# Kernel tuning notes

Hardware: AMD Instinct MI355X
Metric: run time of the kernel (lower is better)

Reference implementation:

```python
import jax, jax.numpy as jnp
import numpy as np

NEG_INF = -1.0e9


def setup_inputs() -> dict:
    key = jax.random.key(0)
    ks = jax.random.split(key, 7)
    B, D, L, N, K = 4096, 512, 20, 8192, 64
    return {
        "inputs_embed": jax.random.normal(ks[0], (B, D), jnp.float32),
        "labels_embed": jax.random.normal(ks[1], (B, D), jnp.float32),
        "labels": jax.random.normal(ks[2], (B, L), jnp.float32),
        "all_labels_embed": jax.random.normal(ks[3], (N, D), jnp.float32),
        "all_labels": jax.random.normal(ks[4], (N, L), jnp.float32),
        "neg_ids_in": jax.random.randint(ks[5], (B, K), 0, B, jnp.int32),
        "neg_ids_lb": jax.random.randint(ks[6], (B, K), 0, N, jnp.int32),
    }


def reference(inputs_embed, labels_embed, labels, all_labels_embed, all_labels,
              neg_ids_in, neg_ids_lb):
    # --- negative sampling (indices supplied; equals tf.gather of tiled table) ---
    neg_ie = inputs_embed[neg_ids_in]        # [B,K,D] negatives from inputs
    neg_le = all_labels_embed[neg_ids_lb]    # [B,K,D] negatives from label table
    # bad-negative masks: negative label features identical to the positive's
    bad_in = jnp.all(labels[neg_ids_in] == labels[:, None, :], axis=-1).astype(inputs_embed.dtype)      # [B,K]
    bad_lb = jnp.all(all_labels[neg_ids_lb] == labels[:, None, :], axis=-1).astype(inputs_embed.dtype)  # [B,K]

    # --- similarities (dot products) ---
    sim_pos = jnp.sum(inputs_embed * labels_embed, axis=-1, keepdims=True)            # [B,1]
    sim_neg_il = jnp.einsum("bd,bkd->bk", inputs_embed, neg_le) + NEG_INF * bad_lb    # [B,K]
    sim_neg_ll = jnp.einsum("bd,bkd->bk", labels_embed, neg_le) + NEG_INF * bad_lb
    sim_neg_ii = jnp.einsum("bd,bkd->bk", inputs_embed, neg_ie) + NEG_INF * bad_in
    sim_neg_li = jnp.einsum("bd,bkd->bk", labels_embed, neg_ie) + NEG_INF * bad_in

    # --- accuracy ---
    max_all = jnp.max(jnp.concatenate([sim_pos, sim_neg_il], axis=-1), axis=-1)
    acc = jnp.mean((max_all == sim_pos[:, 0]).astype(jnp.float32))

    # --- softmax loss, correct class at index 0 ---
    logits = jnp.concatenate([sim_pos, sim_neg_il, sim_neg_ll, sim_neg_ii, sim_neg_li], axis=-1)  # [B,1+4K]
    per_ex = -jax.nn.log_softmax(logits, axis=-1)[:, 0]   # [B]

    # --- confidence-based loss scaling: loss_scale(-per_ex) ---
    q = jnp.exp(-per_ex)
    scale = jnp.where(jnp.max(q) > 0.5,
                      jax.lax.stop_gradient(((1.0 - q) / 0.5) ** 4),
                      jnp.ones_like(q))
    loss = jnp.mean(per_ex * scale)
    return loss, acc
```

## Files before the change

### kernel.cpp

```cpp
#include <hip/hip_runtime.h>
#include <hip/hip_bf16.h>

#define BB 4096
#define DD 512
#define LLAB 20
#define NN 8192
#define KK 64

constexpr float kNegInf = -1.0e9f;
constexpr float kLn2 = 0.69314718055994530942f;
constexpr float kWlPe = 2.5f;
constexpr float kWlTie = 2.0f;

#define OFF_STATS 16384
#define OFF_WL    16640
#define OFF_HLAB  33280
#define OFF_HAL   66048
#define OFF_SIE   131584
#define OFF_SALE  147968
#define OFF_IEQ   180736
#define OFF_ALEQ  (OFF_IEQ + (size_t)BB * DD)
#define WS_NEED   (OFF_ALEQ + (size_t)NN * DD)

__device__ __forceinline__ float dot4(const float4& a, const float4& b) {
  return a.x * b.x + a.y * b.y + a.z * b.z + a.w * b.w;
}

__device__ __forceinline__ float waveReduceSum(float v) {
#pragma unroll
  for (int s = 1; s < 64; s <<= 1) v += __shfl_xor(v, s);
  return v;
}

__device__ __forceinline__ float waveReduceMax(float v) {
#pragma unroll
  for (int s = 1; s < 64; s <<= 1) v = fmaxf(v, __shfl_xor(v, s));
  return v;
}

__device__ __forceinline__ float waveReduceMin(float v) {
#pragma unroll
  for (int s = 1; s < 64; s <<= 1) v = fminf(v, __shfl_xor(v, s));
  return v;
}

__device__ __forceinline__ unsigned long long hash20(const float* __restrict__ p) {
  unsigned long long h = 1469598103934665603ull;
#pragma unroll
  for (int t = 0; t < LLAB; ++t) {
    h ^= (unsigned long long)__float_as_uint(p[t]);
    h *= 1099511628211ull;
  }
  return h;
}

__device__ __forceinline__ int sdot4i(unsigned a, unsigned b, int acc) {
#if __has_builtin(__builtin_amdgcn_sdot4)
  return __builtin_amdgcn_sdot4((int)a, (int)b, acc, false);
#else
#pragma unroll
  for (int t = 0; t < 4; ++t)
    acc += (int)(signed char)(a >> (8 * t)) * (int)(signed char)(b >> (8 * t));
  return acc;
#endif
}

__device__ __forceinline__ unsigned pk4i8(float a, float b, float c, float d, float inv) {
  const int q0 = (int)rintf(a * inv);
  const int q1 = (int)rintf(b * inv);
  const int q2 = (int)rintf(c * inv);
  const int q3 = (int)rintf(d * inv);
  return (q0 & 255) | ((q1 & 255) << 8) | ((q2 & 255) << 16) | ((q3 & 255) << 24);
}

__device__ __forceinline__ float max8abs(const float4& a, const float4& c) {
  return fmaxf(fmaxf(fmaxf(fabsf(a.x), fabsf(a.y)), fmaxf(fabsf(a.z), fabsf(a.w))),
               fmaxf(fmaxf(fabsf(c.x), fabsf(c.y)), fmaxf(fabsf(c.z), fabsf(c.w))));
}

__global__ void init_kernel(unsigned* stats) {
  if (threadIdx.x == 0) {
    stats[0] = 0u;
    stats[1] = 0u;
  }
}

__global__ __launch_bounds__(256) void prep_kernel(
    const float* __restrict__ ie, const float* __restrict__ ale,
    const float* __restrict__ labels, const float* __restrict__ al,
    char* __restrict__ ie_q, char* __restrict__ ale_q,
    float* __restrict__ s_ie, float* __restrict__ s_ale,
    unsigned long long* __restrict__ h_lab,
    unsigned long long* __restrict__ h_al, unsigned* __restrict__ stats) {
  const int tid = threadIdx.x;
  const int lane = tid & 63;
  const int wave = tid >> 6;
  const int w = blockIdx.x * 4 + wave;

  const float* src;
  char* dst;
  float* sc;
  int row;
  if (w < BB) {
    src = ie; dst = ie_q; sc = s_ie; row = w;
  } else {
    src = ale; dst = ale_q; sc = s_ale; row = w - BB;
  }

  const float4* r4 = (const float4*)(src + (size_t)row * DD);
  const float4 a = r4[2 * lane], c = r4[2 * lane + 1];
  float mx = waveReduceMax(max8abs(a, c));
  mx = fmaxf(mx, 1e-20f);
  const float inv = 127.0f / mx;
  uint2 o;
  o.x = pk4i8(a.x, a.y, a.z, a.w, inv);
  o.y = pk4i8(c.x, c.y, c.z, c.w, inv);
  ((uint2*)(dst + (size_t)row * DD))[lane] = o;
  if (lane == 0) sc[row] = mx * (1.0f / 127.0f);

  const int g = blockIdx.x * 256 + tid;
  if (g == 0) {
    stats[0] = 0u;
    stats[1] = 0u;
  }
  if (g < BB) h_lab[g] = hash20(labels + (size_t)g * LLAB);
  else if (g < BB + NN) h_al[g - BB] = hash20(al + (size_t)(g - BB) * LLAB);
}

__global__ __launch_bounds__(256, 4) void row_i8_kernel(
    const float* __restrict__ ie, const float* __restrict__ le,
    const char* __restrict__ ie_q, const char* __restrict__ ale_q,
    const float* __restrict__ s_ie, const float* __restrict__ s_ale,
    const unsigned long long* __restrict__ h_lab,
    const unsigned long long* __restrict__ h_al,
    const int* __restrict__ nin, const int* __restrict__ nlb,
    float* __restrict__ per_ex, int* __restrict__ wl,
    unsigned* __restrict__ stats) {
  const int b = blockIdx.x;
  const int tid = threadIdx.x;
  const int lane = tid & 63;
  const int wave = tid >> 6;
  const int c = lane & 3;
  const int g = lane >> 2;

  __shared__ unsigned qs[2][144];
  __shared__ float qsc[2];
  __shared__ float sims[1 + 4 * KK];
  __shared__ float wred[8];

  const int wuni = __builtin_amdgcn_readfirstlane(wave);
  const int k = wuni * 16 + g;

  const int jl = nlb[b * KK + k];
  const int ji = nin[b * KK + k];
  const unsigned long long hb = h_lab[b];
  const bool bad_lb = (h_al[jl] == hb);
  const bool bad_in = (h_lab[ji] == hb);
  const float sA = s_ale[jl];
  const float sB = s_ie[ji];

  const uint4* arow = (const uint4*)(ale_q + (size_t)jl * DD);
  const uint4* brow = (const uint4*)(ie_q + (size_t)ji * DD);
  uint4 Ar[8], Br[8];
#pragma unroll
  for (int i = 0; i < 8; ++i) {
    Ar[i] = arow[i * 4 + c];
    Br[i] = brow[i * 4 + c];
  }

  if (wave == 0) {
    const float4* ie4 = (const float4*)(ie + (size_t)b * DD);
    const float4* le4 = (const float4*)(le + (size_t)b * DD);
    const float4 qi0 = ie4[2 * lane], qi1 = ie4[2 * lane + 1];
    const float4 ql0 = le4[2 * lane], ql1 = le4[2 * lane + 1];
    float p = dot4(qi0, ql0) + dot4(qi1, ql1);
    p = waveReduceSum(p);
    if (lane == 0) sims[0] = p;
    const float ami = fmaxf(waveReduceMax(max8abs(qi0, qi1)), 1e-20f);
    const float aml = fmaxf(waveReduceMax(max8abs(ql0, ql1)), 1e-20f);
    const float inv_i = 127.0f / ami, inv_l = 127.0f / aml;
    if (lane == 0) {
      qsc[0] = ami * (1.0f / 127.0f);
      qsc[1] = aml * (1.0f / 127.0f);
    }
    const int cw = (lane >> 1) & 3, iw = lane >> 3;
    const int woff = cw * 36 + iw * 4 + (lane & 1) * 2;
    qs[0][woff] = pk4i8(qi0.x, qi0.y, qi0.z, qi0.w, inv_i);
    qs[0][woff + 1] = pk4i8(qi1.x, qi1.y, qi1.z, qi1.w, inv_i);
    qs[1][woff] = pk4i8(ql0.x, ql0.y, ql0.z, ql0.w, inv_l);
    qs[1][woff + 1] = pk4i8(ql1.x, ql1.y, ql1.z, ql1.w, inv_l);
  }
  __syncthreads();

  int il = 0, ll = 0, ii = 0, li = 0;
#pragma unroll
  for (int i = 0; i < 8; ++i) {
    const uint4 qi = *(const uint4*)&qs[0][c * 36 + i * 4];
    const uint4 ql = *(const uint4*)&qs[1][c * 36 + i * 4];
    il = sdot4i(Ar[i].x, qi.x, il); il = sdot4i(Ar[i].y, qi.y, il);
    il = sdot4i(Ar[i].z, qi.z, il); il = sdot4i(Ar[i].w, qi.w, il);
    ll = sdot4i(Ar[i].x, ql.x, ll); ll = sdot4i(Ar[i].y, ql.y, ll);
    ll = sdot4i(Ar[i].z, ql.z, ll); ll = sdot4i(Ar[i].w, ql.w, ll);
    ii = sdot4i(Br[i].x, qi.x, ii); ii = sdot4i(Br[i].y, qi.y, ii);
    ii = sdot4i(Br[i].z, qi.z, ii); ii = sdot4i(Br[i].w, qi.w, ii);
    li = sdot4i(Br[i].x, ql.x, li); li = sdot4i(Br[i].y, ql.y, li);
    li = sdot4i(Br[i].z, ql.z, li); li = sdot4i(Br[i].w, ql.w, li);
  }

  const bool odd = (lane & 1) != 0;
  const int x = odd ? il : ii;
  const int y = odd ? ll : li;
  const int rx = __shfl_xor(x, 1);
  const int ry = __shfl_xor(y, 1);
  const int aa = (odd ? ii : il) + rx;
  const int bb = (odd ? li : ll) + ry;
  const bool hi2 = (lane & 2) != 0;
  const int s1 = hi2 ? aa : bb;
  const int r1 = __shfl_xor(s1, 2);
  const int vi = (hi2 ? bb : aa) + r1;

  const float srow = (c & 1) ? sB : sA;
  const float sq = (c & 2) ? qsc[1] : qsc[0];
  const float v = (float)vi * (srow * sq);
  const bool badf = (c & 1) ? bad_in : bad_lb;
  const float s = badf ? v + kNegInf : v;
  const int slot = ((c & 1) << 1) | (c >> 1);
  sims[1 + slot * KK + k] = s;
  __syncthreads();

  const float vv = sims[1 + tid];
  const float s0 = sims[0];
  float wmax = waveReduceMax(vv);
  if (lane == 0) wred[wave] = wmax;
  __syncthreads();
  float m = fmaxf(fmaxf(wred[0], wred[1]), fmaxf(wred[2], wred[3]));
  m = fmaxf(m, s0);
  const float e = expf(vv - m);
  float wsum = waveReduceSum(e);
  if (lane == 0) wred[4 + wave] = wsum;
  __syncthreads();
  if (tid == 0) {
    const float tot = wred[4] + wred[5] + wred[6] + wred[7] + expf(s0 - m);
    const float pe = m + logf(tot) - s0;
    per_ex[b] = pe;
    const float max_il = wred[0];
    const bool wl_row = (pe < kWlPe) || (fabsf(s0 - max_il) < kWlTie);
    if (wl_row) {
      const unsigned p = atomicAdd(&stats[1], 1u);
      wl[p] = b;
    } else if (s0 >= max_il) {
      atomicAdd(&stats[0], 1u);
    }
  }
}

__device__ __forceinline__ void row_f32_body(
    int b, const float* __restrict__ ie, const float* __restrict__ le,
    const float* __restrict__ labels, const float* __restrict__ ale,
    const float* __restrict__ al, const int* __restrict__ nin,
    const int* __restrict__ nlb, float* __restrict__ per_ex,
    unsigned* __restrict__ stats, bool count_acc, float* sims, float* wred) {
  const int tid = threadIdx.x;
  const int lane = tid & 63;
  const int wave = tid >> 6;

  const float4* ie4 = (const float4*)(ie + (size_t)b * DD);
  const float4* le4 = (const float4*)(le + (size_t)b * DD);
  float4 ier0 = ie4[lane], ier1 = ie4[lane + 64];
  float4 ler0 = le4[lane], ler1 = le4[lane + 64];
  float lab = (lane < LLAB) ? labels[(size_t)b * LLAB + lane] : 0.0f;

  if (wave == 0) {
    float p = dot4(ier0, ler0) + dot4(ier1, ler1);
    p = waveReduceSum(p);
    if (lane == 0) sims[0] = p;
  }

#pragma unroll 2
  for (int kk = 0; kk < KK / 4; ++kk) {
    const int k = wave * (KK / 4) + kk;
    const int j_lb = __builtin_amdgcn_readfirstlane(nlb[(size_t)b * KK + k]);
    const int j_in = __builtin_amdgcn_readfirstlane(nin[(size_t)b * KK + k]);

    const float4* rle = (const float4*)(ale + (size_t)j_lb * DD);
    const float4* rie = (const float4*)(ie + (size_t)j_in * DD);
    float4 vle0 = rle[lane], vle1 = rle[lane + 64];
    float4 vie0 = rie[lane], vie1 = rie[lane + 64];

    bool ein = true, elb = true;
    if (lane < LLAB) {
      ein = (labels[(size_t)j_in * LLAB + lane] == lab);
      elb = (al[(size_t)j_lb * LLAB + lane] == lab);
    }
    const bool bad_in = (__ballot(ein) == ~0ull);
    const bool bad_lb = (__ballot(elb) == ~0ull);

    float a_il = dot4(vle0, ier0) + dot4(vle1, ier1);
    float a_ll = dot4(vle0, ler0) + dot4(vle1, ler1);
    float a_ii = dot4(vie0, ier0) + dot4(vie1, ier1);
    float a_li = dot4(vie0, ler0) + dot4(vie1, ler1);

    const bool oddl = (lane & 1) != 0;
    float sx = oddl ? a_il : a_ii;
    float sy = oddl ? a_ll : a_li;
    float rx = __shfl_xor(sx, 1);
    float ry = __shfl_xor(sy, 1);
    float mx = (oddl ? a_ii : a_il) + rx;
    float my = (oddl ? a_li : a_ll) + ry;
    const bool hi2 = (lane & 2) != 0;
    float s1 = hi2 ? mx : my;
    float r1 = __shfl_xor(s1, 2);
    float v = (hi2 ? my : mx) + r1;
    v += __shfl_xor(v, 4);
    v += __shfl_xor(v, 8);
    v += __shfl_xor(v, 16);
    v += __shfl_xor(v, 32);

    if (lane < 4) {
      const bool badf = (lane & 1) ? bad_in : bad_lb;
      const float s = badf ? v + kNegInf : v;
      const int slot = ((lane & 1) << 1) | ((lane >> 1) & 1);
      sims[1 + slot * KK + k] = s;
    }
  }
  __syncthreads();

  const float v = sims[1 + tid];
  const float s0 = sims[0];
  float wmax = waveReduceMax(v);
  if (lane == 0) wred[wave] = wmax;
  __syncthreads();
  float m = fmaxf(fmaxf(wred[0], wred[1]), fmaxf(wred[2], wred[3]));
  m = fmaxf(m, s0);
  const float e = expf(v - m);
  float wsum = waveReduceSum(e);
  if (lane == 0) wred[4 + wave] = wsum;
  __syncthreads();
  if (tid == 0) {
    const float tot = wred[4] + wred[5] + wred[6] + wred[7] + expf(s0 - m);
    per_ex[b] = m + logf(tot) - s0;
    if (count_acc) {
      const float max_il = wred[0];
      if (s0 >= max_il) atomicAdd(&stats[0], 1u);
    }
  }
}

__global__ __launch_bounds__(256) void row_f32_kernel(
    const float* __restrict__ ie, const float* __restrict__ le,
    const float* __restrict__ labels, const float* __restrict__ ale,
    const float* __restrict__ al, const int* __restrict__ nin,
    const int* __restrict__ nlb, float* __restrict__ per_ex,
    unsigned* __restrict__ stats) {
  __shared__ float sims[1 + 4 * KK];
  __shared__ float wred[8];
  row_f32_body(blockIdx.x, ie, le, labels, ale, al, nin, nlb, per_ex, stats,
               true, sims, wred);
}

__global__ __launch_bounds__(256) void fixup_kernel(
    const float* __restrict__ ie, const float* __restrict__ le,
    const float* __restrict__ labels, const float* __restrict__ ale,
    const float* __restrict__ al, const int* __restrict__ nin,
    const int* __restrict__ nlb, float* __restrict__ per_ex,
    const int* __restrict__ wl, unsigned* __restrict__ stats) {
  __shared__ float sims[1 + 4 * KK];
  __shared__ float wred[8];
  const int n = (int)stats[1];
  for (int w = blockIdx.x; w < n; w += gridDim.x) {
    row_f32_body(wl[w], ie, le, labels, ale, al, nin, nlb, per_ex, stats,
                 true, sims, wred);
    __syncthreads();
  }
}

__global__ __launch_bounds__(256) void finalize_kernel(
    const float* __restrict__ per_ex, const unsigned* __restrict__ stats,
    float* __restrict__ out) {
  __shared__ float pe_s[BB];
  __shared__ float wred[8];
  const int tid = threadIdx.x;
  const int lane = tid & 63;
  const int wave = tid >> 6;

  float mn = 1.0e30f;
#pragma unroll 4
  for (int i = tid; i < BB; i += 256) {
    const float v = per_ex[i];
    pe_s[i] = v;
    mn = fminf(mn, v);
  }
  mn = waveReduceMin(mn);
  if (lane == 0) wred[wave] = mn;
  __syncthreads();
  const float minpe = fminf(fminf(wred[0], wred[1]), fminf(wred[2], wred[3]));
  const bool scale_on = (minpe < kLn2);
  __syncthreads();

  float sum = 0.0f;
#pragma unroll 4
  for (int i = tid; i < BB; i += 256) {
    const float pe = pe_s[i];
    float s = 1.0f;
    if (scale_on) {
      const float q = expf(-pe);
      const float t = 2.0f * (1.0f - q);
      const float t2 = t * t;
      s = t2 * t2;
    }
    sum += pe * s;
  }
  sum = waveReduceSum(sum);
  if (lane == 0) wred[4 + wave] = sum;
  __syncthreads();
  if (tid == 0) {
    const float tot = wred[4] + wred[5] + wred[6] + wred[7];
    out[0] = tot / (float)BB;
    out[1] = (float)stats[0] / (float)BB;
  }
}

extern "C" void kernel_launch(void* const* d_in, const int* in_sizes, int n_in,
                              void* d_out, int out_size, void* d_ws, size_t ws_size,
                              hipStream_t stream) {
  const float* ie = (const float*)d_in[0];
  const float* le = (const float*)d_in[1];
  const float* labels = (const float*)d_in[2];
  const float* ale = (const float*)d_in[3];
  const float* al = (const float*)d_in[4];
  const int* nin = (const int*)d_in[5];
  const int* nlb = (const int*)d_in[6];
  float* out = (float*)d_out;

  float* per_ex = (float*)d_ws;
  unsigned* stats = (unsigned*)((char*)d_ws + OFF_STATS);
  int* wl = (int*)((char*)d_ws + OFF_WL);

  if (ws_size >= WS_NEED) {
    char* ie_q = (char*)d_ws + OFF_IEQ;
    char* ale_q = (char*)d_ws + OFF_ALEQ;
    float* s_ie = (float*)((char*)d_ws + OFF_SIE);
    float* s_ale = (float*)((char*)d_ws + OFF_SALE);
    unsigned long long* h_lab = (unsigned long long*)((char*)d_ws + OFF_HLAB);
    unsigned long long* h_al = (unsigned long long*)((char*)d_ws + OFF_HAL);
    const int prep_blocks = (BB + NN) / 4;
    hipLaunchKernelGGL(prep_kernel, dim3(prep_blocks), dim3(256), 0, stream,
                       ie, ale, labels, al, ie_q, ale_q, s_ie, s_ale,
                       h_lab, h_al, stats);
    hipLaunchKernelGGL(row_i8_kernel, dim3(BB), dim3(256), 0, stream,
                       ie, le, ie_q, ale_q, s_ie, s_ale, h_lab, h_al,
                       nin, nlb, per_ex, wl, stats);
    hipLaunchKernelGGL(fixup_kernel, dim3(64), dim3(256), 0, stream,
                       ie, le, labels, ale, al, nin, nlb, per_ex, wl, stats);
  } else {
    hipLaunchKernelGGL(init_kernel, dim3(1), dim3(64), 0, stream, stats);
    hipLaunchKernelGGL(row_f32_kernel, dim3(BB), dim3(256), 0, stream,
                       ie, le, labels, ale, al, nin, nlb, per_ex, stats);
  }
  hipLaunchKernelGGL(finalize_kernel, dim3(1), dim3(256), 0, stream,
                     per_ex, stats, out);
}
```

Measured before the change: 58.21 us.

## Precompute query quantization in prep and fuse f32 fixup into row kernel

Moves the per-row positive dot product and the int8 quantization of inputs and labels embeddings into the prep kernel, so the row kernel only loads prequantized query rows into shared memory. It also drops one sims shared-memory round trip by reducing max and sum straight from registers. The separate fixup kernel and its worklist atomics go away, and uncertain rows now run the exact f32 path inline within the same block. This saves a launch and a serial tail, but a block that hits the fixup path gets slower and the extra code may raise register pressure in the row kernel.

Result: faster. 53.29 us (-8.5%).

```diff
diff --git a/kernel.cpp b/kernel.cpp
--- a/kernel.cpp
+++ b/kernel.cpp
@@ -13,13 +13,15 @@
 constexpr float kWlTie = 2.0f;
 
 #define OFF_STATS 16384
-#define OFF_WL    16640
-#define OFF_HLAB  33280
-#define OFF_HAL   66048
-#define OFF_SIE   131584
-#define OFF_SALE  147968
-#define OFF_IEQ   180736
-#define OFF_ALEQ  (OFF_IEQ + (size_t)BB * DD)
+#define OFF_SP    16640
+#define OFF_SIE   33024
+#define OFF_SLE   49408
+#define OFF_SALE  65792
+#define OFF_HLAB  98560
+#define OFF_HAL   131328
+#define OFF_IEQ   196864
+#define OFF_LEQ   2294016
+#define OFF_ALEQ  4391168
 #define WS_NEED   (OFF_ALEQ + (size_t)NN * DD)
 
 __device__ __forceinline__ float dot4(const float4& a, const float4& b) {
@@ -79,17 +81,16 @@
 }
 
 __global__ void init_kernel(unsigned* stats) {
-  if (threadIdx.x == 0) {
-    stats[0] = 0u;
-    stats[1] = 0u;
-  }
+  if (threadIdx.x == 0) stats[0] = 0u;
 }
 
 __global__ __launch_bounds__(256) void prep_kernel(
-    const float* __restrict__ ie, const float* __restrict__ ale,
-    const float* __restrict__ labels, const float* __restrict__ al,
-    char* __restrict__ ie_q, char* __restrict__ ale_q,
-    float* __restrict__ s_ie, float* __restrict__ s_ale,
+    const float* __restrict__ ie, const float* __restrict__ le,
+    const float* __restrict__ ale, const float* __restrict__ labels,
+    const float* __restrict__ al, char* __restrict__ ie_q,
+    char* __restrict__ le_q, char* __restrict__ ale_q,
+    float* __restrict__ s_ie, float* __restrict__ s_le,
+    float* __restrict__ s_ale, float* __restrict__ sp,
     unsigned long long* __restrict__ h_lab,
     unsigned long long* __restrict__ h_al, unsigned* __restrict__ stats) {
   const int tid = threadIdx.x;
@@ -97,161 +98,47 @@
   const int wave = tid >> 6;
   const int w = blockIdx.x * 4 + wave;
 
-  const float* src;
-  char* dst;
-  float* sc;
-  int row;
   if (w < BB) {
-    src = ie; dst = ie_q; sc = s_ie; row = w;
+    const float4* i4 = (const float4*)(ie + (size_t)w * DD);
+    const float4* l4 = (const float4*)(le + (size_t)w * DD);
+    const float4 a0 = i4[2 * lane], a1 = i4[2 * lane + 1];
+    const float4 b0 = l4[2 * lane], b1 = l4[2 * lane + 1];
+    float p = dot4(a0, b0) + dot4(a1, b1);
+    p = waveReduceSum(p);
+    float mi = fmaxf(waveReduceMax(max8abs(a0, a1)), 1e-20f);
+    const float inv_i = 127.0f / mi;
+    uint2 oi;
+    oi.x = pk4i8(a0.x, a0.y, a0.z, a0.w, inv_i);
+    oi.y = pk4i8(a1.x, a1.y, a1.z, a1.w, inv_i);
+    ((uint2*)(ie_q + (size_t)w * DD))[lane] = oi;
+    float ml = fmaxf(waveReduceMax(max8abs(b0, b1)), 1e-20f);
+    const float inv_l = 127.0f / ml;
+    uint2 ol;
+    ol.x = pk4i8(b0.x, b0.y, b0.z, b0.w, inv_l);
+    ol.y = pk4i8(b1.x, b1.y, b1.z, b1.w, inv_l);
+    ((uint2*)(le_q + (size_t)w * DD))[lane] = ol;
+    if (lane == 0) {
+      sp[w] = p;
+      s_ie[w] = mi * (1.0f / 127.0f);
+      s_le[w] = ml * (1.0f / 127.0f);
+    }
   } else {
-    src = ale; dst = ale_q; sc = s_ale; row = w - BB;
-  }
-
-  const float4* r4 = (const float4*)(src + (size_t)row * DD);
-  const float4 a = r4[2 * lane], c = r4[2 * lane + 1];
-  float mx = waveReduceMax(max8abs(a, c));
-  mx = fmaxf(mx, 1e-20f);
-  const float inv = 127.0f / mx;
-  uint2 o;
-  o.x = pk4i8(a.x, a.y, a.z, a.w, inv);
-  o.y = pk4i8(c.x, c.y, c.z, c.w, inv);
-  ((uint2*)(dst + (size_t)row * DD))[lane] = o;
-  if (lane == 0) sc[row] = mx * (1.0f / 127.0f);
+    const int row = w - BB;
+    const float4* r4 = (const float4*)(ale + (size_t)row * DD);
+    const float4 a = r4[2 * lane], c = r4[2 * lane + 1];
+    float mx = fmaxf(waveReduceMax(max8abs(a, c)), 1e-20f);
+    const float inv = 127.0f / mx;
+    uint2 o;
+    o.x = pk4i8(a.x, a.y, a.z, a.w, inv);
+    o.y = pk4i8(c.x, c.y, c.z, c.w, inv);
+    ((uint2*)(ale_q + (size_t)row * DD))[lane] = o;
+    if (lane == 0) s_ale[row] = mx * (1.0f / 127.0f);
+  }
 
   const int g = blockIdx.x * 256 + tid;
-  if (g == 0) {
-    stats[0] = 0u;
-    stats[1] = 0u;
-  }
+  if (g == 0) stats[0] = 0u;
   if (g < BB) h_lab[g] = hash20(labels + (size_t)g * LLAB);
   else if (g < BB + NN) h_al[g - BB] = hash20(al + (size_t)(g - BB) * LLAB);
-}
-
-__global__ __launch_bounds__(256, 4) void row_i8_kernel(
-    const float* __restrict__ ie, const float* __restrict__ le,
-    const char* __restrict__ ie_q, const char* __restrict__ ale_q,
-    const float* __restrict__ s_ie, const float* __restrict__ s_ale,
-    const unsigned long long* __restrict__ h_lab,
-    const unsigned long long* __restrict__ h_al,
-    const int* __restrict__ nin, const int* __restrict__ nlb,
-    float* __restrict__ per_ex, int* __restrict__ wl,
-    unsigned* __restrict__ stats) {
-  const int b = blockIdx.x;
-  const int tid = threadIdx.x;
-  const int lane = tid & 63;
-  const int wave = tid >> 6;
-  const int c = lane & 3;
-  const int g = lane >> 2;
-
-  __shared__ unsigned qs[2][144];
-  __shared__ float qsc[2];
-  __shared__ float sims[1 + 4 * KK];
-  __shared__ float wred[8];
-
-  const int wuni = __builtin_amdgcn_readfirstlane(wave);
-  const int k = wuni * 16 + g;
-
-  const int jl = nlb[b * KK + k];
-  const int ji = nin[b * KK + k];
-  const unsigned long long hb = h_lab[b];
-  const bool bad_lb = (h_al[jl] == hb);
-  const bool bad_in = (h_lab[ji] == hb);
-  const float sA = s_ale[jl];
-  const float sB = s_ie[ji];
-
-  const uint4* arow = (const uint4*)(ale_q + (size_t)jl * DD);
-  const uint4* brow = (const uint4*)(ie_q + (size_t)ji * DD);
-  uint4 Ar[8], Br[8];
-#pragma unroll
-  for (int i = 0; i < 8; ++i) {
-    Ar[i] = arow[i * 4 + c];
-    Br[i] = brow[i * 4 + c];
-  }
-
-  if (wave == 0) {
-    const float4* ie4 = (const float4*)(ie + (size_t)b * DD);
-    const float4* le4 = (const float4*)(le + (size_t)b * DD);
-    const float4 qi0 = ie4[2 * lane], qi1 = ie4[2 * lane + 1];
-    const float4 ql0 = le4[2 * lane], ql1 = le4[2 * lane + 1];
-    float p = dot4(qi0, ql0) + dot4(qi1, ql1);
-    p = waveReduceSum(p);
-    if (lane == 0) sims[0] = p;
-    const float ami = fmaxf(waveReduceMax(max8abs(qi0, qi1)), 1e-20f);
-    const float aml = fmaxf(waveReduceMax(max8abs(ql0, ql1)), 1e-20f);
-    const float inv_i = 127.0f / ami, inv_l = 127.0f / aml;
-    if (lane == 0) {
-      qsc[0] = ami * (1.0f / 127.0f);
-      qsc[1] = aml * (1.0f / 127.0f);
-    }
-    const int cw = (lane >> 1) & 3, iw = lane >> 3;
-    const int woff = cw * 36 + iw * 4 + (lane & 1) * 2;
-    qs[0][woff] = pk4i8(qi0.x, qi0.y, qi0.z, qi0.w, inv_i);
-    qs[0][woff + 1] = pk4i8(qi1.x, qi1.y, qi1.z, qi1.w, inv_i);
-    qs[1][woff] = pk4i8(ql0.x, ql0.y, ql0.z, ql0.w, inv_l);
-    qs[1][woff + 1] = pk4i8(ql1.x, ql1.y, ql1.z, ql1.w, inv_l);
-  }
-  __syncthreads();
-
-  int il = 0, ll = 0, ii = 0, li = 0;
-#pragma unroll
-  for (int i = 0; i < 8; ++i) {
-    const uint4 qi = *(const uint4*)&qs[0][c * 36 + i * 4];
-    const uint4 ql = *(const uint4*)&qs[1][c * 36 + i * 4];
-    il = sdot4i(Ar[i].x, qi.x, il); il = sdot4i(Ar[i].y, qi.y, il);
-    il = sdot4i(Ar[i].z, qi.z, il); il = sdot4i(Ar[i].w, qi.w, il);
-    ll = sdot4i(Ar[i].x, ql.x, ll); ll = sdot4i(Ar[i].y, ql.y, ll);
-    ll = sdot4i(Ar[i].z, ql.z, ll); ll = sdot4i(Ar[i].w, ql.w, ll);
-    ii = sdot4i(Br[i].x, qi.x, ii); ii = sdot4i(Br[i].y, qi.y, ii);
-    ii = sdot4i(Br[i].z, qi.z, ii); ii = sdot4i(Br[i].w, qi.w, ii);
-    li = sdot4i(Br[i].x, ql.x, li); li = sdot4i(Br[i].y, ql.y, li);
-    li = sdot4i(Br[i].z, ql.z, li); li = sdot4i(Br[i].w, ql.w, li);
-  }
-
-  const bool odd = (lane & 1) != 0;
-  const int x = odd ? il : ii;
-  const int y = odd ? ll : li;
-  const int rx = __shfl_xor(x, 1);
-  const int ry = __shfl_xor(y, 1);
-  const int aa = (odd ? ii : il) + rx;
-  const int bb = (odd ? li : ll) + ry;
-  const bool hi2 = (lane & 2) != 0;
-  const int s1 = hi2 ? aa : bb;
-  const int r1 = __shfl_xor(s1, 2);
-  const int vi = (hi2 ? bb : aa) + r1;
-
-  const float srow = (c & 1) ? sB : sA;
-  const float sq = (c & 2) ? qsc[1] : qsc[0];
-  const float v = (float)vi * (srow * sq);
-  const bool badf = (c & 1) ? bad_in : bad_lb;
-  const float s = badf ? v + kNegInf : v;
-  const int slot = ((c & 1) << 1) | (c >> 1);
-  sims[1 + slot * KK + k] = s;
-  __syncthreads();
-
-  const float vv = sims[1 + tid];
-  const float s0 = sims[0];
-  float wmax = waveReduceMax(vv);
-  if (lane == 0) wred[wave] = wmax;
-  __syncthreads();
-  float m = fmaxf(fmaxf(wred[0], wred[1]), fmaxf(wred[2], wred[3]));
-  m = fmaxf(m, s0);
-  const float e = expf(vv - m);
-  float wsum = waveReduceSum(e);
-  if (lane == 0) wred[4 + wave] = wsum;
-  __syncthreads();
-  if (tid == 0) {
-    const float tot = wred[4] + wred[5] + wred[6] + wred[7] + expf(s0 - m);
-    const float pe = m + logf(tot) - s0;
-    per_ex[b] = pe;
-    const float max_il = wred[0];
-    const bool wl_row = (pe < kWlPe) || (fabsf(s0 - max_il) < kWlTie);
-    if (wl_row) {
-      const unsigned p = atomicAdd(&stats[1], 1u);
-      wl[p] = b;
-    } else if (s0 >= max_il) {
-      atomicAdd(&stats[0], 1u);
-    }
-  }
 }
 
 __device__ __forceinline__ void row_f32_body(
@@ -346,6 +233,119 @@
   }
 }
 
+__global__ __launch_bounds__(256, 4) void row_i8_kernel(
+    const float* __restrict__ ie, const float* __restrict__ le,
+    const float* __restrict__ labels, const float* __restrict__ ale,
+    const float* __restrict__ al, const char* __restrict__ ie_q,
+    const char* __restrict__ le_q, const char* __restrict__ ale_q,
+    const float* __restrict__ s_ie, const float* __restrict__ s_le,
+    const float* __restrict__ s_ale, const float* __restrict__ sp,
+    const unsigned long long* __restrict__ h_lab,
+    const unsigned long long* __restrict__ h_al,
+    const int* __restrict__ nin, const int* __restrict__ nlb,
+    float* __restrict__ per_ex, unsigned* __restrict__ stats) {
+  const int b = blockIdx.x;
+  const int tid = threadIdx.x;
+  const int lane = tid & 63;
+  const int wave = tid >> 6;
+  const int c = lane & 3;
+  const int g = lane >> 2;
+
+  __shared__ uint4 qls4[64];
+  __shared__ float simsX[1 + 4 * KK];
+  __shared__ float wred[12];
+  __shared__ int do_fix;
+
+  const int wuni = __builtin_amdgcn_readfirstlane(wave);
+  const int k = wuni * 16 + g;
+
+  const int jl = nlb[b * KK + k];
+  const int ji = nin[b * KK + k];
+  const unsigned long long hb = h_lab[b];
+  const bool bad_lb = (h_al[jl] == hb);
+  const bool bad_in = (h_lab[ji] == hb);
+  const float sA = s_ale[jl];
+  const float sB = s_ie[ji];
+
+  const uint4* arow = (const uint4*)(ale_q + (size_t)jl * DD);
+  const uint4* brow = (const uint4*)(ie_q + (size_t)ji * DD);
+  uint4 Ar[8], Br[8];
+#pragma unroll
+  for (int i = 0; i < 8; ++i) {
+    Ar[i] = arow[i * 4 + c];
+    Br[i] = brow[i * 4 + c];
+  }
+
+  if (wave == 0) {
+    if (lane < 32) qls4[lane] = ((const uint4*)(ie_q + (size_t)b * DD))[lane];
+    else qls4[lane] = ((const uint4*)(le_q + (size_t)b * DD))[lane - 32];
+  }
+  __syncthreads();
+
+  int il = 0, ll = 0, ii = 0, li = 0;
+#pragma unroll
+  for (int i = 0; i < 8; ++i) {
+    const uint4 qi = qls4[i * 4 + c];
+    const uint4 ql = qls4[32 + i * 4 + c];
+    il = sdot4i(Ar[i].x, qi.x, il); il = sdot4i(Ar[i].y, qi.y, il);
+    il = sdot4i(Ar[i].z, qi.z, il); il = sdot4i(Ar[i].w, qi.w, il);
+    ll = sdot4i(Ar[i].x, ql.x, ll); ll = sdot4i(Ar[i].y, ql.y, ll);
+    ll = sdot4i(Ar[i].z, ql.z, ll); ll = sdot4i(Ar[i].w, ql.w, ll);
+    ii = sdot4i(Br[i].x, qi.x, ii); ii = sdot4i(Br[i].y, qi.y, ii);
+    ii = sdot4i(Br[i].z, qi.z, ii); ii = sdot4i(Br[i].w, qi.w, ii);
+    li = sdot4i(Br[i].x, ql.x, li); li = sdot4i(Br[i].y, ql.y, li);
+    li = sdot4i(Br[i].z, ql.z, li); li = sdot4i(Br[i].w, ql.w, li);
+  }
+
+  const bool odd = (lane & 1) != 0;
+  const int x = odd ? il : ii;
+  const int y = odd ? ll : li;
+  const int rx = __shfl_xor(x, 1);
+  const int ry = __shfl_xor(y, 1);
+  const int aa = (odd ? ii : il) + rx;
+  const int bb2 = (odd ? li : ll) + ry;
+  const bool hi2 = (lane & 2) != 0;
+  const int s1 = hi2 ? aa : bb2;
+  const int r1 = __shfl_xor(s1, 2);
+  const int vi = (hi2 ? bb2 : aa) + r1;
+
+  const float srow = (c & 1) ? sB : sA;
+  const float sq = (c & 2) ? s_le[b] : s_ie[b];
+  const float v = (float)vi * (srow * sq);
+  const bool badf = (c & 1) ? bad_in : bad_lb;
+  const float s = badf ? v + kNegInf : v;
+
+  const float s0 = sp[b];
+
+  float m_w = waveReduceMax(s);
+  float mil_w = waveReduceMax((c == 0) ? s : -3.0e38f);
+  if (lane == 0) {
+    wred[wave] = m_w;
+    wred[4 + wave] = mil_w;
+  }
+  __syncthreads();
+  float m = fmaxf(fmaxf(fmaxf(wred[0], wred[1]), fmaxf(wred[2], wred[3])), s0);
+  const float e = expf(s - m);
+  float sum_w = waveReduceSum(e);
+  if (lane == 0) wred[8 + wave] = sum_w;
+  __syncthreads();
+  if (tid == 0) {
+    const float tot = wred[8] + wred[9] + wred[10] + wred[11] + expf(s0 - m);
+    const float pe = m + logf(tot) - s0;
+    per_ex[b] = pe;
+    const float max_il = fmaxf(fmaxf(wred[4], wred[5]), fmaxf(wred[6], wred[7]));
+    const bool wl_row = (pe < kWlPe) || (fabsf(s0 - max_il) < kWlTie);
+    do_fix = wl_row ? 1 : 0;
+    if (!wl_row && s0 >= max_il) atomicAdd(&stats[0], 1u);
+  }
+  __syncthreads();
+
+  if (do_fix) {
+    row_f32_body(b, ie, le, labels, ale, al, nin, nlb, per_ex, stats,
+                 true, simsX, wred);
+  }
+}
+
 __global__ __launch_bounds__(256) void row_f32_kernel(
     const float* __restrict__ ie, const float* __restrict__ le,
     const float* __restrict__ labels, const float* __restrict__ ale,
@@ -356,22 +356,6 @@
   __shared__ float wred[8];
   row_f32_body(blockIdx.x, ie, le, labels, ale, al, nin, nlb, per_ex, stats,
                true, sims, wred);
-}
-
-__global__ __launch_bounds__(256) void fixup_kernel(
-    const float* __restrict__ ie, const float* __restrict__ le,
-    const float* __restrict__ labels, const float* __restrict__ ale,
-    const float* __restrict__ al, const int* __restrict__ nin,
-    const int* __restrict__ nlb, float* __restrict__ per_ex,
-    const int* __restrict__ wl, unsigned* __restrict__ stats) {
-  __shared__ float sims[1 + 4 * KK];
-  __shared__ float wred[8];
-  const int n = (int)stats[1];
-  for (int w = blockIdx.x; w < n; w += gridDim.x) {
-    row_f32_body(wl[w], ie, le, labels, ale, al, nin, nlb, per_ex, stats,
-                 true, sims, wred);
-    __syncthreads();
-  }
 }
 
 __global__ __launch_bounds__(256) void finalize_kernel(
@@ -434,24 +418,25 @@
 
   float* per_ex = (float*)d_ws;
   unsigned* stats = (unsigned*)((char*)d_ws + OFF_STATS);
-  int* wl = (int*)((char*)d_ws + OFF_WL);
 
   if (ws_size >= WS_NEED) {
     char* ie_q = (char*)d_ws + OFF_IEQ;
+    char* le_q = (char*)d_ws + OFF_LEQ;
     char* ale_q = (char*)d_ws + OFF_ALEQ;
     float* s_ie = (float*)((char*)d_ws + OFF_SIE);
+    float* s_le = (float*)((char*)d_ws + OFF_SLE);
     float* s_ale = (float*)((char*)d_ws + OFF_SALE);
+    float* sp = (float*)((char*)d_ws + OFF_SP);
     unsigned long long* h_lab = (unsigned long long*)((char*)d_ws + OFF_HLAB);
     unsigned long long* h_al = (unsigned long long*)((char*)d_ws + OFF_HAL);
     const int prep_blocks = (BB + NN) / 4;
     hipLaunchKernelGGL(prep_kernel, dim3(prep_blocks), dim3(256), 0, stream,
-                       ie, ale, labels, al, ie_q, ale_q, s_ie, s_ale,
-                       h_lab, h_al, stats);
+                       ie, le, ale, labels, al, ie_q, le_q, ale_q,
+                       s_ie, s_le, s_ale, sp, h_lab, h_al, stats);
     hipLaunchKernelGGL(row_i8_kernel, dim3(BB), dim3(256), 0, stream,
-                       ie, le, ie_q, ale_q, s_ie, s_ale, h_lab, h_al,
-                       nin, nlb, per_ex, wl, stats);
-    hipLaunchKernelGGL(fixup_kernel, dim3(64), dim3(256), 0, stream,
-                       ie, le, labels, ale, al, nin, nlb, per_ex, wl, stats);
+                       ie, le, labels, ale, al, ie_q, le_q, ale_q,
+                       s_ie, s_le, s_ale, sp, h_lab, h_al, nin, nlb,
+                       per_ex, stats);
   } else {
     hipLaunchKernelGGL(init_kernel, dim3(1), dim3(64), 0, stream, stats);
     hipLaunchKernelGGL(row_f32_kernel, dim3(BB), dim3(256), 0, stream,
```
